# Performance work log

Measured on AMD Instinct MI355X. Metric: run time of the kernel, lower is better.

The kernel has to match this reference:

```python
import jax, jax.numpy as jnp
import numpy as np

EPS_BN = 1e-3  # nn.BatchNorm1d(num_channels, eps=0.001)
B, C, N = 16, 256, 2048
NUM_SA = 4


def _bn(x, g, b, m, v):
    # eval-mode BatchNorm1d over channel dim of [B, C, N]
    return g[:, None] * (x - m[:, None]) * jax.lax.rsqrt(v[:, None] + EPS_BN) + b[:, None]


def _sa_layer(x, qk_w, v_w, v_b, t_w, t_b, g, b, m, var):
    # q_conv and k_conv share weights -> energy = (Wx)^T (Wx)
    q = jnp.einsum('oc,bcn->bon', qk_w, x)              # [B, C//4, N]
    energy = jnp.einsum('bcm,bcn->bmn', q, q)           # [B, N, N]
    attn = jax.nn.softmax(energy, axis=-1)
    # offset-attention: extra column-sum normalization (dim=1)
    attn = attn / (1e-9 + attn.sum(axis=1, keepdims=True))
    xv = jnp.einsum('oc,bcn->bon', v_w, x) + v_b[:, None]   # [B, C, N]
    x_r = jnp.einsum('bcn,bnm->bcm', xv, attn)              # bmm(x_v, attention)
    t = jnp.einsum('oc,bcn->bon', t_w, x - x_r) + t_b[:, None]
    return x + jax.nn.relu(_bn(t, g, b, m, var))


def setup_inputs() -> dict:
    key = jax.random.key(0)
    ks = jax.random.split(key, 24)
    f32 = jnp.float32
    d = {}
    d['x'] = jax.random.normal(ks[0], (B, C, N), dtype=f32)
    d['conv1_w'] = jax.random.normal(ks[1], (C, C), dtype=f32) * 0.05
    d['conv2_w'] = jax.random.normal(ks[2], (C, C), dtype=f32) * 0.05
    for i, nm in enumerate(['bn1', 'bn2']):
        kk = jax.random.split(ks[3 + i], 4)
        d[nm + '_g'] = 1.0 + 0.05 * jax.random.normal(kk[0], (C,), dtype=f32)
        d[nm + '_b'] = 0.05 * jax.random.normal(kk[1], (C,), dtype=f32)
        d[nm + '_m'] = 0.05 * jax.random.normal(kk[2], (C,), dtype=f32)
        d[nm + '_v'] = jax.random.uniform(kk[3], (C,), dtype=f32, minval=0.5, maxval=1.5)
    d['sa_qk_w'] = jax.random.normal(ks[5], (NUM_SA, C // 4, C), dtype=f32) * 0.05
    d['sa_v_w'] = jax.random.normal(ks[6], (NUM_SA, C, C), dtype=f32) * 0.05
    d['sa_v_b'] = jax.random.normal(ks[7], (NUM_SA, C), dtype=f32) * 0.05
    d['sa_t_w'] = jax.random.normal(ks[8], (NUM_SA, C, C), dtype=f32) * 0.05
    d['sa_t_b'] = jax.random.normal(ks[9], (NUM_SA, C), dtype=f32) * 0.05
    d['sa_g'] = 1.0 + 0.05 * jax.random.normal(ks[10], (NUM_SA, C), dtype=f32)
    d['sa_b'] = 0.05 * jax.random.normal(ks[11], (NUM_SA, C), dtype=f32)
    d['sa_m'] = 0.05 * jax.random.normal(ks[12], (NUM_SA, C), dtype=f32)
    d['sa_var'] = jax.random.uniform(ks[13], (NUM_SA, C), dtype=f32, minval=0.5, maxval=1.5)
    d['flag'] = 0  # False -> primary bn branch
    return d


def reference(x, conv1_w, conv2_w, bn1_g, bn1_b, bn1_m, bn1_v,
              bn2_g, bn2_b, bn2_m, bn2_v,
              sa_qk_w, sa_v_w, sa_v_b, sa_t_w, sa_t_b,
              sa_g, sa_b, sa_m, sa_var, flag):
    h = jax.nn.relu(_bn(jnp.einsum('oc,bcn->bon', conv1_w, x), bn1_g, bn1_b, bn1_m, bn1_v))
    h = jax.nn.relu(_bn(jnp.einsum('oc,bcn->bon', conv2_w, h), bn2_g, bn2_b, bn2_m, bn2_v))
    outs = []
    for i in range(NUM_SA):
        h = _sa_layer(h, sa_qk_w[i], sa_v_w[i], sa_v_b[i], sa_t_w[i], sa_t_b[i],
                      sa_g[i], sa_b[i], sa_m[i], sa_var[i])
        outs.append(h)
    return jnp.concatenate(outs, axis=1)  # [B, 4*C, N]
```

## Files before the change

### kernel.cpp

```cpp
#include <hip/hip_runtime.h>
#include <hip/hip_bf16.h>
#include <hip/hip_fp16.h>

static constexpr int Bn = 16;
static constexpr int Cc = 256;
static constexpr int Nn = 2048;
static constexpr int C4 = 64;
static constexpr float LOG2E = 1.4426950408889634f;

typedef _Float16 half_t;
typedef __attribute__((ext_vector_type(8))) _Float16 half8;
typedef __attribute__((ext_vector_type(4))) _Float16 half4;
typedef __attribute__((ext_vector_type(8))) short short8;
typedef __attribute__((ext_vector_type(4))) float float4v;

static constexpr long sNC = (long)Nn * Cc;
static constexpr long sNQ = (long)Nn * C4;

#define DEVI __device__ __forceinline__

DEVI float bf2f(unsigned short u) { return __uint_as_float(((unsigned)u) << 16); }
DEVI unsigned short f2bf(float f) {
    unsigned x = __float_as_uint(f);
    x += 0x7fffu + ((x >> 16) & 1u);
    return (unsigned short)(x >> 16);
}

DEVI void gload16(const void* g, void* l) {
    __builtin_amdgcn_global_load_lds(
        (const __attribute__((address_space(1))) unsigned int*)g,
        (__attribute__((address_space(3))) unsigned int*)l, 16, 0, 0);
}

enum { EPI_RAW = 0, EPI_H = 1, EPI_XV = 2 };

template<int MODE, int BM, int BN, int WI, int WJ, bool BF16OUT>
__global__ __launch_bounds__(WI * WJ * 64)
void mgemm(const half_t* __restrict__ A, long aB,
           const half_t* __restrict__ Bm, long bB,
           void* __restrict__ Yv, long yB, int ldy,
           const float* __restrict__ bias,
           const float* __restrict__ bng, const float* __restrict__ bnb,
           const float* __restrict__ bnm, const float* __restrict__ bnv,
           int K,
           const float* __restrict__ Pbuf, float* __restrict__ offp)
{
    constexpr int NW = WI * WJ;
    __shared__ __align__(16) half_t Als[2][BM][32];
    __shared__ __align__(16) half_t Bls[2][BN][32];

    const int tid  = threadIdx.x;
    const int w    = tid >> 6;
    const int lane = tid & 63;
    const int wi   = w % WI;
    const int wj   = w / WI;
    const int quad = lane >> 4, m16 = lane & 15;
    const int lr   = lane >> 2, lc = lane & 3;
    const int b    = blockIdx.z;
    const int j0   = blockIdx.x * BN;
    const int i0   = blockIdx.y * BM;

    const half_t* Ab = A + (size_t)b * aB;
    const half_t* Bb = Bm + (size_t)b * bB;

    float4v acc[4][4];
    #pragma unroll
    for (int i = 0; i < 4; ++i)
        #pragma unroll
        for (int j = 0; j < 4; ++j) acc[i][j] = (float4v)0.f;

    bool first = true;
    for (int k0 = 0; k0 < K; k0 += 64) {
        #pragma unroll
        for (int s = 0; s < 2; ++s) {
            const int kk = k0 + s * 32 + lc * 8;
            #pragma unroll
            for (int t = 0; t < BM / (16 * NW); ++t) {
                const int row = (t * NW + w) * 16;
                gload16(Ab + (size_t)(i0 + row + lr) * K + kk, &Als[s][row][0]);
            }
            #pragma unroll
            for (int t = 0; t < BN / (16 * NW); ++t) {
                const int row = (t * NW + w) * 16;
                gload16(Bb + (size_t)(j0 + row + lr) * K + kk, &Bls[s][row][0]);
            }
        }
        if (MODE == EPI_XV && first && Pbuf && tid < 128) {
            const int m = blockIdx.y * 128 + tid;
            const float2* p = (const float2*)(Pbuf + ((size_t)b * Nn + m) * 32);
            float M = -1e30f;
            #pragma unroll
            for (int i = 0; i < 16; ++i) M = fmaxf(M, p[i].x);
            float S = 0.f;
            #pragma unroll
            for (int i = 0; i < 16; ++i) S += p[i].y * __expf(p[i].x - M);
            offp[(size_t)b * Nn + m] = fmaf(M, LOG2E, __log2f(S));
        }
        first = false;
        __syncthreads();
        #pragma unroll
        for (int s = 0; s < 2; ++s) {
            half8 af[4], bf[4];
            #pragma unroll
            for (int t = 0; t < 4; ++t)
                af[t] = *(const half8*)&Als[s][wi * 64 + t * 16 + m16][quad * 8];
            #pragma unroll
            for (int t = 0; t < 4; ++t)
                bf[t] = *(const half8*)&Bls[s][wj * 64 + t * 16 + m16][quad * 8];
            #pragma unroll
            for (int ti = 0; ti < 4; ++ti)
                #pragma unroll
                for (int tj = 0; tj < 4; ++tj)
                    acc[ti][tj] = __builtin_amdgcn_mfma_f32_16x16x32_f16(
                        af[ti], bf[tj], acc[ti][tj], 0, 0, 0);
        }
        __syncthreads();
    }

    #pragma unroll
    for (int ti = 0; ti < 4; ++ti) {
        const int il = i0 + wi * 64 + ti * 16 + quad * 4;
        #pragma unroll
        for (int tj = 0; tj < 4; ++tj) {
            const int jl = j0 + wj * 64 + tj * 16 + m16;
            float4v v = acc[ti][tj];
            if (MODE == EPI_RAW) {
                half4 o;
                #pragma unroll
                for (int r = 0; r < 4; ++r) o[r] = (half_t)v[r];
                *(half4*)((half_t*)Yv + (size_t)b * yB + (size_t)jl * ldy + il) = o;
            } else if (MODE == EPI_H) {
                half4 o;
                #pragma unroll
                for (int r = 0; r < 4; ++r) {
                    const float sc = bng[il + r] * rsqrtf(bnv[il + r] + 1e-3f);
                    const float sh = bnb[il + r] - bnm[il + r] * sc;
                    o[r] = (half_t)fmaxf(fmaf(v[r], sc, sh), 0.f);
                }
                *(half4*)((half_t*)Yv + (size_t)b * yB + (size_t)jl * ldy + il) = o;
            } else {
                const float bj = bias[jl];
                if (BF16OUT) {
                    ushort4 o;
                    o.x = f2bf(v[0] + bj); o.y = f2bf(v[1] + bj);
                    o.z = f2bf(v[2] + bj); o.w = f2bf(v[3] + bj);
                    *(ushort4*)((unsigned short*)Yv + (size_t)b * yB + (size_t)jl * ldy + il) = o;
                } else {
                    half4 o;
                    #pragma unroll
                    for (int r = 0; r < 4; ++r) o[r] = (half_t)(v[r] + bj);
                    *(half4*)((half_t*)Yv + (size_t)b * yB + (size_t)jl * ldy + il) = o;
                }
            }
        }
    }
}

__global__ __launch_bounds__(256)
void estats(const half_t* __restrict__ q, float* __restrict__ Pbuf)
{
    __shared__ __align__(16) half_t sA[128 * 64];
    __shared__ __align__(16) half_t sB[128 * 64];
    __shared__ float red[2][2][4][16][2];
    const int tid = threadIdx.x, w = tid >> 6, lane = tid & 63;
    const int wi = w & 1, wj = w >> 1, quad = lane >> 4, m16 = lane & 15;
    const int f = blockIdx.x;
    const int W = (f & 7) * 512 + (f >> 3);
    const int b = W >> 8;
    const int rem = W & 255;
    const int j0 = (rem & 15) * 128;
    const int ib = rem >> 4;
    const int i0 = ib * 128;
    const half_t* qb = q + (size_t)b * sNQ;

    #pragma unroll
    for (int t = 0; t < 4; ++t) {
        const int g = w * 256 + t * 64 + lane;
        const int r = g >> 3, c = g & 7;
        const int cs = c ^ (r & 7);
        gload16(qb + (size_t)(i0 + r) * 64 + cs * 8, sA + (w * 256 + t * 64) * 8);
        gload16(qb + (size_t)(j0 + r) * 64 + cs * 8, sB + (w * 256 + t * 64) * 8);
    }
    __syncthreads();

    half8 an[4][2], bm[4][2];
    #pragma unroll
    for (int t = 0; t < 4; ++t)
        #pragma unroll
        for (int ks = 0; ks < 2; ++ks) {
            const int pc = ((ks * 4 + quad) ^ (m16 & 7)) * 8;
            an[t][ks] = *(const half8*)&sA[(wi * 64 + t * 16 + m16) * 64 + pc];
            bm[t][ks] = *(const half8*)&sB[(wj * 64 + t * 16 + m16) * 64 + pc];
        }

    #pragma unroll
    for (int tj = 0; tj < 4; ++tj) {
        float4v e[4];
        #pragma unroll
        for (int ti = 0; ti < 4; ++ti) {
            e[ti] = (float4v)0.f;
            e[ti] = __builtin_amdgcn_mfma_f32_16x16x32_f16(an[ti][0], bm[tj][0], e[ti], 0, 0, 0);
            e[ti] = __builtin_amdgcn_mfma_f32_16x16x32_f16(an[ti][1], bm[tj][1], e[ti], 0, 0, 0);
        }
        float lmax = -1e30f;
        #pragma unroll
        for (int ti = 0; ti < 4; ++ti)
            #pragma unroll
            for (int r = 0; r < 4; ++r) lmax = fmaxf(lmax, e[ti][r]);
        lmax = fmaxf(lmax, __shfl_xor(lmax, 16));
        lmax = fmaxf(lmax, __shfl_xor(lmax, 32));
        float ls = 0.f;
        #pragma unroll
        for (int ti = 0; ti < 4; ++ti)
            #pragma unroll
            for (int r = 0; r < 4; ++r) ls += __expf(e[ti][r] - lmax);
        ls += __shfl_xor(ls, 16);
        ls += __shfl_xor(ls, 32);
        if (quad == 0) { red[wi][wj][tj][m16][0] = lmax; red[wi][wj][tj][m16][1] = ls; }
    }
    __syncthreads();
    if (tid < 128) {
        const int wj2 = tid >> 6, tj2 = (tid >> 4) & 3, mm = tid & 15;
        const float m0 = red[0][wj2][tj2][mm][0], s0 = red[0][wj2][tj2][mm][1];
        const float m1 = red[1][wj2][tj2][mm][0], s1 = red[1][wj2][tj2][mm][1];
        const float M = fmaxf(m0, m1);
        const float S = s0 * __expf(m0 - M) + s1 * __expf(m1 - M);
        const int m = j0 + wj2 * 64 + tj2 * 16 + mm;
        *(float2*)(Pbuf + (((size_t)b * Nn + m) * 16 + ib) * 2) = make_float2(M, S);
    }
}

__global__ __launch_bounds__(512)
void flashxr(const half_t* __restrict__ q, const half_t* __restrict__ xv,
             const half_t* __restrict__ h, const float* __restrict__ offp,
             const half_t* __restrict__ tw, const float* __restrict__ tb,
             const float* __restrict__ bng, const float* __restrict__ bnb,
             const float* __restrict__ bnm, const float* __restrict__ bnv,
             float* __restrict__ outL, half_t* __restrict__ hNext)
{
    __shared__ __align__(16) half_t sXV[256 * 64];
    __shared__ __align__(16) half_t sQA[2][64 * 64];
    __shared__ __align__(16) half_t sP[64 * 64];
    __shared__ float sOff[Nn];

    const int tid = threadIdx.x, w = tid >> 6, lane = tid & 63;
    const int quad = lane >> 4, m16 = lane & 15;
    const int wiE = w & 1, wjE = w >> 1;
    const int wi = w & 3, wj = w >> 2;
    const int wjT = w;
    const int f = blockIdx.x;
    const int W = (f & 7) * 64 + (f >> 3);
    const int b = W >> 5, j0 = (W & 31) * 64;
    const half_t* qb  = q + (size_t)b * sNQ;
    const half_t* xvb = xv + (size_t)b * sNC;

    const int sr = tid >> 3, sc = tid & 7;
    const int qsw = (sc ^ (sr & 7)) * 8;

    gload16(qb + (size_t)sr * 64 + qsw, &sQA[0][(size_t)tid * 8]);
    gload16(offp + (size_t)b * Nn + (size_t)tid * 4, sOff + (size_t)tid * 4);

    half8 bq[2];
    #pragma unroll
    for (int s = 0; s < 2; ++s)
        bq[s] = *(const half8*)(qb + (size_t)(j0 + wjE * 16 + m16) * 64 + (s * 4 + quad) * 8);

    __syncthreads();

    float4v acc[4][2];
    #pragma unroll
    for (int i = 0; i < 4; ++i)
        #pragma unroll
        for (int j = 0; j < 2; ++j) acc[i][j] = (float4v)0.f;
    float csa = 0.f;
    const int mrow = wjE * 16 + m16;

    for (int nc = 0; nc < 32; ++nc) {
        #pragma unroll
        for (int t = 0; t < 4; ++t) {
            const int g = t * 512 + tid;
            const int r = g >> 3, c = g & 7;
            gload16(xvb + (size_t)r * Nn + nc * 64 + ((c ^ (r & 7)) * 8),
                    sXV + (size_t)g * 8);
        }
        if (nc < 31)
            gload16(qb + (size_t)((nc + 1) * 64 + sr) * 64 + qsw,
                    &sQA[(nc + 1) & 1][(size_t)tid * 8]);
        __syncthreads();

        const half_t* qA = &sQA[nc & 1][0];
        const int nbase = nc * 64 + wiE * 32 + quad * 4;
        #pragma unroll
        for (int ti = 0; ti < 2; ++ti) {
            const int nl = wiE * 32 + ti * 16 + m16;
            const half8 an0 = *(const half8*)&qA[(size_t)nl * 64 + ((quad ^ (m16 & 7)) * 8)];
            const half8 an1 = *(const half8*)&qA[(size_t)nl * 64 + (((4 + quad) ^ (m16 & 7)) * 8)];
            float4v e = (float4v)0.f;
            e = __builtin_amdgcn_mfma_f32_16x16x32_f16(an0, bq[0], e, 0, 0, 0);
            e = __builtin_amdgcn_mfma_f32_16x16x32_f16(an1, bq[1], e, 0, 0, 0);
            const float4v o4 = *(const float4v*)&sOff[nbase + ti * 16];
            float c0 = 0.f; ushort4 pk;
            #pragma unroll
            for (int r = 0; r < 4; ++r) {
                const float p = __builtin_amdgcn_exp2f(fmaf(e[r], LOG2E, -o4[r]));
                c0 += p; (&pk.x)[r] = f2bf(p);
            }
            csa += c0;
            const int pc = (wiE * 4 + ti * 2 + (quad >> 1)) ^ (m16 & 7);
            *(ushort4*)&((unsigned short*)sP)[(size_t)mrow * 64 + pc * 8 + (quad & 1) * 4] = pk;
        }
        __syncthreads();

        #pragma unroll
        for (int ks = 0; ks < 2; ++ks) {
            short8 xa[4], pb[2];
            #pragma unroll
            for (int ti = 0; ti < 4; ++ti)
                xa[ti] = *(const short8*)&sXV[(size_t)(wi * 64 + ti * 16 + m16) * 64
                                              + (((ks * 4 + quad) ^ (m16 & 7)) * 8)];
            #pragma unroll
            for (int tj = 0; tj < 2; ++tj)
                pb[tj] = *(const short8*)&sP[(size_t)(wj * 32 + tj * 16 + m16) * 64
                                             + (((ks * 4 + quad) ^ (m16 & 7)) * 8)];
            __builtin_amdgcn_s_setprio(1);
            #pragma unroll
            for (int ti = 0; ti < 4; ++ti)
                #pragma unroll
                for (int tj = 0; tj < 2; ++tj)
                    acc[ti][tj] = __builtin_amdgcn_mfma_f32_16x16x32_bf16(
                        xa[ti], pb[tj], acc[ti][tj], 0, 0, 0);
            __builtin_amdgcn_s_setprio(0);
        }
        __syncthreads();
    }

    csa += __shfl_xor(csa, 16);
    csa += __shfl_xor(csa, 32);
    float* fb = (float*)sP;
    if (lane < 16) fb[wiE * 64 + wjE * 16 + lane] = csa;
    __syncthreads();
    float csr[2];
    #pragma unroll
    for (int tj = 0; tj < 2; ++tj) {
        const int m = wj * 32 + tj * 16 + m16;
        csr[tj] = 1.0f / (1e-9f + fb[m] + fb[64 + m]);
    }

    const half_t* hb = h + (size_t)b * sNC;
    half_t* sD = sXV;
    #pragma unroll
    for (int ti = 0; ti < 4; ++ti) {
        const int cg = wi * 64 + ti * 16 + quad * 4;
        const int cc = (cg >> 3) ^ (m16 & 7);
        const int sub = (quad & 1) * 4;
        #pragma unroll
        for (int tj = 0; tj < 2; ++tj) {
            const int mr = wj * 32 + tj * 16 + m16;
            const int mg = j0 + mr;
            const half4 hv = *(const half4*)&hb[(size_t)mg * Cc + cg];
            half4 o;
            #pragma unroll
            for (int r = 0; r < 4; ++r)
                o[r] = (half_t)((float)hv[r] - acc[ti][tj][r] * csr[tj]);
            *(half4*)&sD[(size_t)mr * 256 + cc * 8 + sub] = o;
        }
    }
    __syncthreads();

    float4v acc2[4][2];
    #pragma unroll
    for (int i = 0; i < 4; ++i)
        #pragma unroll
        for (int j = 0; j < 2; ++j) acc2[i][j] = (float4v)0.f;
    #pragma unroll
    for (int ks = 0; ks < 8; ++ks) {
        half8 af[4], bf[2];
        #pragma unroll
        for (int tm = 0; tm < 4; ++tm)
            af[tm] = *(const half8*)&sD[(size_t)(tm * 16 + m16) * 256
                                        + (((ks * 4 + quad) ^ (m16 & 7)) * 8)];
        #pragma unroll
        for (int tc = 0; tc < 2; ++tc)
            bf[tc] = *(const half8*)&tw[(size_t)(wjT * 32 + tc * 16 + m16) * 256
                                        + ks * 32 + quad * 8];
        #pragma unroll
        for (int tm = 0; tm < 4; ++tm)
            #pragma unroll
            for (int tc = 0; tc < 2; ++tc)
                acc2[tm][tc] = __builtin_amdgcn_mfma_f32_16x16x32_f16(
                    af[tm], bf[tc], acc2[tm][tc], 0, 0, 0);
    }

    const long yB = (long)4 * Cc * Nn;
    float* yb = outL + (size_t)b * yB;
    half_t* hn = hNext ? hNext + (size_t)b * sNC : nullptr;
    #pragma unroll
    for (int tc = 0; tc < 2; ++tc) {
        const int co = wjT * 32 + tc * 16 + m16;
        const float tb2 = tb[co];
        const float sc2 = bng[co] * rsqrtf(bnv[co] + 1e-3f);
        const float sh2 = bnb[co] - bnm[co] * sc2;
        #pragma unroll
        for (int tm = 0; tm < 4; ++tm) {
            const int mg = j0 + tm * 16 + quad * 4;
            float4v o;
            #pragma unroll
            for (int r = 0; r < 4; ++r) {
                const float t2  = acc2[tm][tc][r] + tb2;
                const float rel = fmaxf(fmaf(t2, sc2, sh2), 0.f);
                const float hv  = (float)hb[(size_t)(mg + r) * Cc + co];
                const float ov  = hv + rel;
                o[r] = ov;
                if (hn) hn[(size_t)(mg + r) * Cc + co] = (half_t)ov;
            }
            *(float4v*)&yb[(size_t)co * Nn + mg] = o;
        }
    }
}

__global__ __launch_bounds__(256)
void xpose_cast(const float* __restrict__ x, half_t* __restrict__ xT)
{
    __shared__ half_t tile[32][33];
    const int tx = threadIdx.x & 31, ty = threadIdx.x >> 5;
    const int n0 = blockIdx.x * 32, c0 = blockIdx.y * 32, b = blockIdx.z;
    #pragma unroll
    for (int r = 0; r < 4; ++r)
        tile[ty * 4 + r][tx] =
            (half_t)x[((size_t)b * Cc + c0 + ty * 4 + r) * Nn + n0 + tx];
    __syncthreads();
    #pragma unroll
    for (int r = 0; r < 4; ++r)
        xT[((size_t)b * Nn + n0 + ty * 4 + r) * Cc + c0 + tx] = tile[tx][ty * 4 + r];
}

__global__ __launch_bounds__(256)
void castall(const float* __restrict__ c1, const float* __restrict__ c2,
             const float* __restrict__ qk, const float* __restrict__ vw,
             const float* __restrict__ tw, half_t* __restrict__ dst)
{
    const int i = (blockIdx.x * 256 + threadIdx.x) * 4;
    const float* s; int o;
    if      (i < 65536)  { s = c1; o = 0; }
    else if (i < 131072) { s = c2; o = 65536; }
    else if (i < 196608) { s = qk; o = 131072; }
    else if (i < 458752) { s = vw; o = 196608; }
    else                 { s = tw; o = 458752; }
    const float4v v = *(const float4v*)(s + (i - o));
    half4 out;
    #pragma unroll
    for (int r = 0; r < 4; ++r) out[r] = (half_t)v[r];
    *(half4*)(dst + i) = out;
}

extern "C" void kernel_launch(void* const* d_in, const int* in_sizes, int n_in,
                              void* d_out, int out_size, void* d_ws, size_t ws_size,
                              hipStream_t stream)
{
    const float* x    = (const float*)d_in[0];
    const float* c1w  = (const float*)d_in[1];
    const float* c2w  = (const float*)d_in[2];
    const float* bn1g = (const float*)d_in[3], *bn1b = (const float*)d_in[4];
    const float* bn1m = (const float*)d_in[5], *bn1v = (const float*)d_in[6];
    const float* bn2g = (const float*)d_in[7], *bn2b = (const float*)d_in[8];
    const float* bn2m = (const float*)d_in[9], *bn2v = (const float*)d_in[10];
    const float* qkw  = (const float*)d_in[11];
    const float* vw   = (const float*)d_in[12];
    const float* vb   = (const float*)d_in[13];
    const float* tw   = (const float*)d_in[14];
    const float* tb   = (const float*)d_in[15];
    const float* sag  = (const float*)d_in[16];
    const float* sab  = (const float*)d_in[17];
    const float* sam  = (const float*)d_in[18];
    const float* sav  = (const float*)d_in[19];
    float* out = (float*)d_out;

    char* ws = (char*)d_ws;
    const size_t HSZ = (size_t)Bn * Nn * Cc * 2;
    half_t* xT   = (half_t*)(ws);
    half_t* hA   = (half_t*)(ws + HSZ);
    half_t* hBuf = (half_t*)(ws + 2 * HSZ);
    half_t* q_s  = (half_t*)(ws + 3 * HSZ);
    half_t* xv_s = (half_t*)(ws + 3 * HSZ + (size_t)4194304);
    float*  Pbuf = (float*) (ws + 4 * HSZ + (size_t)4194304);
    float*  offp = (float*) (ws + 4 * HSZ + (size_t)8388608);
    half_t* warena = (half_t*)(ws + 4 * HSZ + (size_t)8519680);
    half_t* wc1  = warena;
    half_t* wc2  = wc1 + 65536;
    half_t* wqk  = wc2 + 65536;
    half_t* wv   = wqk + 65536;
    half_t* wt   = wv  + 262144;

    dim3 blk(256);

    castall<<<768, blk, 0, stream>>>(c1w, c2w, qkw, vw, tw, warena);
    xpose_cast<<<dim3(Nn / 32, Cc / 32, Bn), blk, 0, stream>>>(x, xT);

    mgemm<EPI_H, 256, 128, 4, 2, false><<<dim3(16, 1, Bn), dim3(512), 0, stream>>>(
        wc1, 0, xT, sNC, hA, sNC, Cc,
        nullptr, bn1g, bn1b, bn1m, bn1v, Cc, nullptr, nullptr);
    mgemm<EPI_H, 256, 128, 4, 2, false><<<dim3(16, 1, Bn), dim3(512), 0, stream>>>(
        wc2, 0, hA, sNC, hBuf, sNC, Cc,
        nullptr, bn2g, bn2b, bn2m, bn2v, Cc, nullptr, nullptr);

    half_t* hcur = hBuf;
    half_t* hnxt = hA;
    for (int L = 0; L < 4; ++L) {
        mgemm<EPI_RAW, 64, 256, 1, 4, false><<<dim3(8, 1, Bn), blk, 0, stream>>>(
            wqk + (long)L * C4 * Cc, 0, hcur, sNC, q_s, sNQ, C4,
            nullptr, nullptr, nullptr, nullptr, nullptr, Cc, nullptr, nullptr);
        estats<<<dim3(4096), blk, 0, stream>>>(q_s, Pbuf);
        mgemm<EPI_XV, 128, 256, 2, 4, true><<<dim3(1, 16, Bn), dim3(512), 0, stream>>>(
            hcur, sNC, wv + (long)L * Cc * Cc, 0, xv_s, (long)Cc * Nn, Nn,
            vb + L * Cc, nullptr, nullptr, nullptr, nullptr, Cc, Pbuf, offp);
        flashxr<<<dim3(512), dim3(512), 0, stream>>>(
            q_s, xv_s, hcur, offp,
            wt + (long)L * Cc * Cc, tb + L * Cc,
            sag + L * Cc, sab + L * Cc, sam + L * Cc, sav + L * Cc,
            out + (long)L * Cc * Nn, (L < 3) ? hnxt : nullptr);
        half_t* tmp = hcur; hcur = hnxt; hnxt = tmp;
    }
}
```

Before: 677.4 us.

## Fuse next layer's q projection into flashxr epilogue

Measured after the change: 671.5 us. About the same (-0.9%).

```diff
diff --git a/kernel.cpp b/kernel.cpp
--- a/kernel.cpp
+++ b/kernel.cpp
@@ -236,7 +236,8 @@
              const half_t* __restrict__ tw, const float* __restrict__ tb,
              const float* __restrict__ bng, const float* __restrict__ bnb,
              const float* __restrict__ bnm, const float* __restrict__ bnv,
-             float* __restrict__ outL, half_t* __restrict__ hNext)
+             float* __restrict__ outL, half_t* __restrict__ hNext,
+             const half_t* __restrict__ qkn, half_t* __restrict__ qn)
 {
     __shared__ __align__(16) half_t sXV[256 * 64];
     __shared__ __align__(16) half_t sQA[2][64 * 64];
@@ -391,6 +392,9 @@
                     af[tm], bf[tc], acc2[tm][tc], 0, 0, 0);
     }
 
+    if (qn) __syncthreads();
+
+    half_t* sH = sXV;
     const long yB = (long)4 * Cc * Nn;
     float* yb = outL + (size_t)b * yB;
     half_t* hn = hNext ? hNext + (size_t)b * sNC : nullptr;
@@ -412,9 +416,40 @@
                 const float ov  = hv + rel;
                 o[r] = ov;
                 if (hn) hn[(size_t)(mg + r) * Cc + co] = (half_t)ov;
+                if (qn) {
+                    const int row = tm * 16 + quad * 4 + r;
+                    const int chk = ((co >> 3) ^ (row & 7));
+                    sH[(size_t)row * 256 + chk * 8 + (co & 7)] = (half_t)ov;
+                }
             }
             *(float4v*)&yb[(size_t)co * Nn + mg] = o;
         }
+    }
+
+    if (qn) {
+        __syncthreads();
+        const int ot = w & 3;
+        const int mt0 = (w >> 2) * 2;
+        float4v acc3[2];
+        acc3[0] = (float4v)0.f; acc3[1] = (float4v)0.f;
+        #pragma unroll
+        for (int ks = 0; ks < 8; ++ks) {
+            const half8 bf = *(const half8*)&qkn[(size_t)(ot * 16 + m16) * 256
+                                                + ks * 32 + quad * 8];
+            #pragma unroll
+            for (int mi = 0; mi < 2; ++mi) {
+                const half8 af = *(const half8*)&sH[(size_t)((mt0 + mi) * 16 + m16) * 256
+                                                    + (((ks * 4 + quad) ^ (m16 & 7)) * 8)];
+                acc3[mi] = __builtin_amdgcn_mfma_f32_16x16x32_f16(af, bf, acc3[mi], 0, 0, 0);
+            }
+        }
+        half_t* qnb = qn + (size_t)b * sNQ;
+        #pragma unroll
+        for (int mi = 0; mi < 2; ++mi)
+            #pragma unroll
+            for (int r = 0; r < 4; ++r)
+                qnb[(size_t)(j0 + (mt0 + mi) * 16 + quad * 4 + r) * 64
+                    + ot * 16 + m16] = (half_t)acc3[mi][r];
     }
 }
 
@@ -480,11 +515,12 @@
     half_t* xT   = (half_t*)(ws);
     half_t* hA   = (half_t*)(ws + HSZ);
     half_t* hBuf = (half_t*)(ws + 2 * HSZ);
-    half_t* q_s  = (half_t*)(ws + 3 * HSZ);
+    half_t* q_sA = (half_t*)(ws + 3 * HSZ);
     half_t* xv_s = (half_t*)(ws + 3 * HSZ + (size_t)4194304);
     float*  Pbuf = (float*) (ws + 4 * HSZ + (size_t)4194304);
     float*  offp = (float*) (ws + 4 * HSZ + (size_t)8388608);
     half_t* warena = (half_t*)(ws + 4 * HSZ + (size_t)8519680);
+    half_t* q_sB = (half_t*)(ws + 4 * HSZ + (size_t)8519680 + (size_t)2097152);
     half_t* wc1  = warena;
     half_t* wc2  = wc1 + 65536;
     half_t* wqk  = wc2 + 65536;
@@ -503,21 +539,27 @@
         wc2, 0, hA, sNC, hBuf, sNC, Cc,
         nullptr, bn2g, bn2b, bn2m, bn2v, Cc, nullptr, nullptr);
 
+    mgemm<EPI_RAW, 64, 256, 1, 4, false><<<dim3(8, 1, Bn), blk, 0, stream>>>(
+        wqk, 0, hBuf, sNC, q_sA, sNQ, C4,
+        nullptr, nullptr, nullptr, nullptr, nullptr, Cc, nullptr, nullptr);
+
     half_t* hcur = hBuf;
     half_t* hnxt = hA;
+    half_t* qcur = q_sA;
+    half_t* qnxt = q_sB;
     for (int L = 0; L < 4; ++L) {
-        mgemm<EPI_RAW, 64, 256, 1, 4, false><<<dim3(8, 1, Bn), blk, 0, stream>>>(
-            wqk + (long)L * C4 * Cc, 0, hcur, sNC, q_s, sNQ, C4,
-            nullptr, nullptr, nullptr, nullptr, nullptr, Cc, nullptr, nullptr);
-        estats<<<dim3(4096), blk, 0, stream>>>(q_s, Pbuf);
+        estats<<<dim3(4096), blk, 0, stream>>>(qcur, Pbuf);
         mgemm<EPI_XV, 128, 256, 2, 4, true><<<dim3(1, 16, Bn), dim3(512), 0, stream>>>(
             hcur, sNC, wv + (long)L * Cc * Cc, 0, xv_s, (long)Cc * Nn, Nn,
             vb + L * Cc, nullptr, nullptr, nullptr, nullptr, Cc, Pbuf, offp);
         flashxr<<<dim3(512), dim3(512), 0, stream>>>(
-            q_s, xv_s, hcur, offp,
+            qcur, xv_s, hcur, offp,
             wt + (long)L * Cc * Cc, tb + L * Cc,
             sag + L * Cc, sab + L * Cc, sam + L * Cc, sav + L * Cc,
-            out + (long)L * Cc * Nn, (L < 3) ? hnxt : nullptr);
+            out + (long)L * Cc * Nn, (L < 3) ? hnxt : nullptr,
+            wqk + (long)(L + 1 < 4 ? L + 1 : 0) * C4 * Cc,
+            (L < 3) ? qnxt : nullptr);
         half_t* tmp = hcur; hcur = hnxt; hnxt = tmp;
-    }
-}
+        half_t* tq  = qcur; qcur = qnxt; qnxt = tq;
+    }
+}
```
